# Kernel tuning notes

Measured on AMD Instinct MI355X. Metric: run time of the kernel, lower is better.

## Reference

```python
import jax, jax.numpy as jnp
import numpy as np

N, E, D, H, DH, M = 100000, 1600000, 128, 8, 16, 3  # nodes, edges, model_dim, heads, head_dim, views
NEG = -1e9


def setup_inputs() -> dict:
    key = jax.random.key(0)
    ks = jax.random.split(key, 12)
    x = jax.random.normal(ks[0], (N, D), jnp.float32)
    src = jax.random.randint(ks[1], (E,), 0, N)
    dst = jax.random.randint(ks[2], (E,), 0, N)
    pi = jax.random.uniform(ks[3], (N, H, M), jnp.float32)
    pi = pi / pi.sum(-1, keepdims=True)  # router mixture over views
    view_w = jax.random.uniform(ks[4], (E, M), jnp.float32)
    s = 1.0 / np.sqrt(D)
    Wq = jax.random.normal(ks[5], (D, D), jnp.float32) * s
    Wk = jax.random.normal(ks[6], (D, D), jnp.float32) * s
    Wv = jax.random.normal(ks[7], (D, D), jnp.float32) * s
    bq = jax.random.normal(ks[8], (D,), jnp.float32) * 0.02
    bk = jax.random.normal(ks[9], (D,), jnp.float32) * 0.02
    bv = jax.random.normal(ks[10], (D,), jnp.float32) * 0.02
    return {"x": x, "pi": pi, "view_w": view_w, "Wq": Wq, "bq": bq,
            "Wk": Wk, "bk": bk, "Wv": Wv, "bv": bv, "src": src, "dst": dst}


def reference(x, pi, view_w, Wq, bq, Wk, bk, Wv, bv, src, dst):
    n = x.shape[0]
    q = (x @ Wq + bq).reshape(n, H, DH)
    k = (x @ Wk + bk).reshape(n, H, DH)
    v = (x @ Wv + bv).reshape(n, H, DH)
    # per-edge mixture weight: sum over views of pi[dst] * view_w  -> [E, H]
    mix = jnp.einsum('ehm,em->eh', pi[dst], view_w)
    raw = jnp.einsum('ehd,ehd->eh', q[dst], k[src]) / jnp.sqrt(jnp.float32(DH))
    scores = raw + jnp.log(jnp.clip(mix, 1e-8))  # adjacency_mode == 'bias'
    valid = mix > 0
    masked = jnp.where(valid, scores, NEG)
    # scatter-softmax over incoming edges per (node, head)
    smax = jax.ops.segment_max(masked, dst, num_segments=n)
    expv = jnp.where(valid, jnp.exp(masked - smax[dst]), 0.0)
    ssum = jax.ops.segment_sum(expv, dst, num_segments=n)
    attn = expv / jnp.maximum(ssum[dst], 1e-8)  # [E, H]
    # weighted scatter-sum aggregation -> [N, H, DH]
    node_states = jax.ops.segment_sum(v[src] * attn[:, :, None], dst, num_segments=n)
    return node_states, attn
```

## Files before the change

kernel.cpp:

```cpp
#include <hip/hip_runtime.h>
#include <hip/hip_bf16.h>
#include <math.h>

#define SCAN_CHUNK 2048

typedef _Float16 half2v __attribute__((ext_vector_type(2)));
typedef _Float16 half8 __attribute__((ext_vector_type(8)));
typedef float floatx4 __attribute__((ext_vector_type(4)));

#if defined(__has_builtin)
#if __has_builtin(__builtin_amdgcn_fdot2)
#define USE_FDOT2 1
#endif
#endif


__global__ void hist_kernel(const int* __restrict__ dst, int* __restrict__ counts, int e) {
    int i = blockIdx.x * blockDim.x + threadIdx.x;
    if (i < e) atomicAdd(&counts[dst[i]], 1);
}

__global__ __launch_bounds__(256) void scan_block_sums(const int* __restrict__ counts,
                                                       int* __restrict__ bsum, int n) {
    __shared__ int sd[256];
    int t = threadIdx.x;
    int base = blockIdx.x * SCAN_CHUNK + t * 8;
    int s = 0;
#pragma unroll
    for (int j = 0; j < 8; ++j) {
        int idx = base + j;
        if (idx < n) s += counts[idx];
    }
    sd[t] = s;
    __syncthreads();
    for (int off = 128; off > 0; off >>= 1) {
        if (t < off) sd[t] += sd[t + off];
        __syncthreads();
    }
    if (t == 0) bsum[blockIdx.x] = sd[0];
}

__global__ void scan_wave(int* bsum, int nb) {
    int lane = threadIdx.x;
    int orig = (lane < nb) ? bsum[lane] : 0;
    int v = orig;
    for (int off = 1; off < 64; off <<= 1) {
        int t = __shfl_up(v, off, 64);
        if (lane >= off) v += t;
    }
    if (lane < nb) bsum[lane] = v - orig;
}

__global__ __launch_bounds__(256) void scan_write(const int* __restrict__ counts,
                                                  const int* __restrict__ bsum,
                                                  int* __restrict__ row_ptr,
                                                  int* __restrict__ cursor,
                                                  int n, int total) {
    __shared__ int sd[256];
    int t = threadIdx.x;
    int base = blockIdx.x * SCAN_CHUNK + t * 8;
    int v[8];
    int s = 0;
#pragma unroll
    for (int j = 0; j < 8; ++j) {
        int idx = base + j;
        v[j] = (idx < n) ? counts[idx] : 0;
        s += v[j];
    }
    sd[t] = s;
    __syncthreads();
    for (int off = 1; off < 256; off <<= 1) {
        int tmp = 0;
        if (t >= off) tmp = sd[t - off];
        __syncthreads();
        if (t >= off) sd[t] += tmp;
        __syncthreads();
    }
    int run = bsum[blockIdx.x] + sd[t] - s;
#pragma unroll
    for (int j = 0; j < 8; ++j) {
        int idx = base + j;
        if (idx < n) {
            row_ptr[idx] = run;
            cursor[idx] = run;
            run += v[j];
        }
    }
    if (blockIdx.x == 0 && t == 0) row_ptr[n] = total;
}

__global__ void fill_csr(const int* __restrict__ dst, const int* __restrict__ src,
                         const float* __restrict__ vw, int* cursor,
                         int4* __restrict__ recs, int* __restrict__ pos, int e) {
    int i = blockIdx.x * blockDim.x + threadIdx.x;
    if (i < e) {
        int p = atomicAdd(&cursor[dst[i]], 1);
        float w0 = vw[3 * i], w1 = vw[3 * i + 1], w2 = vw[3 * i + 2];
        unsigned u0 = (unsigned)__builtin_bit_cast(unsigned short, (_Float16)w0);
        unsigned u1 = (unsigned)__builtin_bit_cast(unsigned short, (_Float16)w1);
        unsigned u2 = (unsigned)__builtin_bit_cast(unsigned short, (_Float16)w2);
        int4 r;
        r.x = src[i];
        r.y = (int)u2;
        r.z = (int)(u0 | (u1 << 16));
        r.w = 0;
        recs[p] = r;
        pos[i] = p;
    }
}


__global__ __launch_bounds__(256) void convert_x(const float* __restrict__ x,
                                                 _Float16* __restrict__ xh, int total8) {
    int i = blockIdx.x * blockDim.x + threadIdx.x;
    if (i < total8) {
        const float4* s = (const float4*)x + i * 2;
        float4 a = s[0], b = s[1];
        half8 h;
        h[0] = (_Float16)a.x; h[1] = (_Float16)a.y; h[2] = (_Float16)a.z; h[3] = (_Float16)a.w;
        h[4] = (_Float16)b.x; h[5] = (_Float16)b.y; h[6] = (_Float16)b.z; h[7] = (_Float16)b.w;
        *((half8*)xh + i) = h;
    }
}

__global__ __launch_bounds__(256) void prep_w(const float* __restrict__ Wq,
                                              const float* __restrict__ Wk,
                                              const float* __restrict__ Wv,
                                              _Float16* __restrict__ wt) {
    const float* W = (blockIdx.x == 0) ? Wq : (blockIdx.x == 1) ? Wk : Wv;
    _Float16* out = wt + (size_t)blockIdx.x * 16384;
    int t = threadIdx.x;
    for (int r = 0; r < 64; ++r) {
        int idx = r * 256 + t;
        int k = idx >> 7, nn = idx & 127;
        out[nn * 128 + k] = (_Float16)W[idx];
    }
}


#define LDP 136

__global__ __launch_bounds__(256) void qkv_mfma(
    const _Float16* __restrict__ xh, const _Float16* __restrict__ wt,
    const float* __restrict__ bq, const float* __restrict__ bk,
    const float* __restrict__ bv,
    _Float16* __restrict__ qh, _Float16* __restrict__ kh, _Float16* __restrict__ vh,
    int n) {
    __shared__ __align__(16) _Float16 xs[128 * LDP];
    __shared__ __align__(16) _Float16 ws[128 * LDP];

    int t = threadIdx.x;
    int tile0 = blockIdx.x * 128;
    int sel = blockIdx.y;
    const _Float16* wsel = wt + (size_t)sel * 16384;
    const float* bias = (sel == 0) ? bq : (sel == 1) ? bk : bv;
    _Float16* out = (sel == 0) ? qh : (sel == 1) ? kh : vh;

#pragma unroll
    for (int r = 0; r < 8; ++r) {
        int id = r * 256 + t;
        int row = id >> 4, c8 = id & 15;
        int grow = tile0 + row;
        half8 val = (half8)(_Float16)0;
        if (grow < n) val = *((const half8*)(xh + (size_t)grow * 128) + c8);
        *((half8*)(xs + row * LDP) + c8) = val;
        half8 wv = *((const half8*)(wsel + row * 128) + c8);
        *((half8*)(ws + row * LDP) + c8) = wv;
    }
    __syncthreads();

    int wave = t >> 6, lane = t & 63;
    int wm = (wave & 1) * 64, wn = (wave >> 1) * 64;
    int lrow = lane & 15, quad = lane >> 4;

    floatx4 acc[4][4];
#pragma unroll
    for (int i = 0; i < 4; ++i)
#pragma unroll
        for (int j = 0; j < 4; ++j) acc[i][j] = (floatx4)0.f;

#pragma unroll
    for (int kk = 0; kk < 4; ++kk) {
        int kbase = kk * 32 + quad * 8;
        half8 a[4], b[4];
#pragma unroll
        for (int i = 0; i < 4; ++i)
            a[i] = *(const half8*)(xs + (wm + i * 16 + lrow) * LDP + kbase);
#pragma unroll
        for (int j = 0; j < 4; ++j)
            b[j] = *(const half8*)(ws + (wn + j * 16 + lrow) * LDP + kbase);
#pragma unroll
        for (int i = 0; i < 4; ++i)
#pragma unroll
            for (int j = 0; j < 4; ++j)
                acc[i][j] = __builtin_amdgcn_mfma_f32_16x16x32_f16(a[i], b[j], acc[i][j], 0, 0, 0);
    }

#pragma unroll
    for (int i = 0; i < 4; ++i) {
#pragma unroll
        for (int j = 0; j < 4; ++j) {
            int col = wn + j * 16 + lrow;
            float bv_ = bias[col];
#pragma unroll
            for (int r = 0; r < 4; ++r) {
                int row = wm + i * 16 + quad * 4 + r;
                int grow = tile0 + row;
                if (grow < n) out[(size_t)grow * 128 + col] = (_Float16)(acc[i][j][r] + bv_);
            }
        }
    }
}


#define STAGE_META(S, idx)                                                    \
    {                                                                         \
        s##S = 0; m##S = 0.f;                                                 \
        if ((idx) < end) {                                                    \
            int4 r_ = recs[(idx)];                                            \
            s##S = r_.x;                                                      \
            half2v w01_ = __builtin_bit_cast(half2v, r_.z);                   \
            _Float16 w2_ =                                                    \
                __builtin_bit_cast(_Float16, (unsigned short)(unsigned)r_.y); \
            m##S = fmaf(p0, (float)w01_[0],                                   \
                        fmaf(p1, (float)w01_[1], p2 * (float)w2_));           \
        }                                                                     \
    }

#define ISSUE_KV(S, idx)                                                      \
    {                                                                         \
        k##S = (half8)(_Float16)0; v##S = (half8)(_Float16)0;                 \
        if ((idx) < end) {                                                    \
            k##S = *(const half8*)(kbase + (size_t)s##S * 128);               \
            v##S = *(const half8*)(vbase + (size_t)s##S * 128);               \
        }                                                                     \
    }

#ifdef USE_FDOT2
#define DOT8(dres, kS)                                                        \
    {                                                                         \
        _Pragma("unroll")                                                     \
        for (int jj_ = 0; jj_ < 4; ++jj_) {                                   \
            half2v x_, y_;                                                    \
            x_[0] = qv[2 * jj_]; x_[1] = qv[2 * jj_ + 1];                     \
            y_[0] = kS[2 * jj_]; y_[1] = kS[2 * jj_ + 1];                     \
            dres = __builtin_amdgcn_fdot2(x_, y_, dres, false);               \
        }                                                                     \
    }
#else
#define DOT8(dres, kS)                                                        \
    {                                                                         \
        _Pragma("unroll")                                                     \
        for (int jj_ = 0; jj_ < 8; ++jj_)                                     \
            dres = fmaf((float)qv[jj_], (float)kS[jj_], dres);                \
    }
#endif

#define COMPUTE(S, mx, slot, validc)                                          \
    {                                                                         \
        float d_ = 0.f;                                                       \
        DOT8(d_, k##S);                                                       \
        d_ += __shfl_xor(d_, 1, 64);                                          \
        float p_ = ((mx) > 0.f) ? (mx)*__expf(d_ * 0.25f) : 0.f;              \
        if (sub == 0 && (validc)) pbuf[(size_t)(slot)*8 + h] = (_Float16)p_;  \
        l += p_;                                                              \
        a0 = fmaf(p_, (float)v##S[0], a0);                                    \
        a1 = fmaf(p_, (float)v##S[1], a1);                                    \
        a2 = fmaf(p_, (float)v##S[2], a2);                                    \
        a3 = fmaf(p_, (float)v##S[3], a3);                                    \
        a4 = fmaf(p_, (float)v##S[4], a4);                                    \
        a5 = fmaf(p_, (float)v##S[5], a5);                                    \
        a6 = fmaf(p_, (float)v##S[6], a6);                                    \
        a7 = fmaf(p_, (float)v##S[7], a7);                                    \
    }

#define BODY(S0, S1, S2, S3, jj)                                              \
    {                                                                         \
        ISSUE_KV(S2, (jj) + 2);                                               \
        ISSUE_KV(S3, (jj) + 3);                                               \
        float mx0_ = m##S0, mx1_ = m##S1;                                     \
        STAGE_META(S0, (jj) + 4);                                             \
        STAGE_META(S1, (jj) + 5);                                             \
        COMPUTE(S0, mx0_, (jj), true);                                        \
        COMPUTE(S1, mx1_, (jj) + 1, (jj) + 1 < end);                          \
    }

__global__ __launch_bounds__(64, 6) void edge_attn(
    const _Float16* __restrict__ qh, const _Float16* __restrict__ kh,
    const _Float16* __restrict__ vh, const float* __restrict__ pi,
    const int* __restrict__ row_ptr, const int4* __restrict__ recs,
    float* __restrict__ node_out, float* __restrict__ invb,
    _Float16* __restrict__ pbuf, int n) {
    int t = threadIdx.x;
    int node = blockIdx.x * 4 + (t >> 4);
    if (node >= n) return;
    int q16 = t & 15;
    int h = q16 >> 1, sub = q16 & 1;
    int off = h * 16 + sub * 8;

    const half8 qv = *(const half8*)(qh + (size_t)node * 128 + off);
    const _Float16* kbase = kh + off;
    const _Float16* vbase = vh + off;

    float p0 = pi[node * 24 + h * 3 + 0];
    float p1 = pi[node * 24 + h * 3 + 1];
    float p2 = pi[node * 24 + h * 3 + 2];
    int beg = row_ptr[node], end = row_ptr[node + 1];

    float l = 0.f;
    float a0 = 0.f, a1 = 0.f, a2 = 0.f, a3 = 0.f;
    float a4 = 0.f, a5 = 0.f, a6 = 0.f, a7 = 0.f;

    int sA, sB, sC, sD;
    float mA, mB, mC, mD;
    half8 kA, vA, kB, vB, kC, vC, kD, vD;

    STAGE_META(A, beg);
    STAGE_META(B, beg + 1);
    STAGE_META(C, beg + 2);
    STAGE_META(D, beg + 3);
    ISSUE_KV(A, beg);
    ISSUE_KV(B, beg + 1);

    for (int j = beg; j < end;) {
        BODY(A, B, C, D, j);
        j += 2;
        if (j >= end) break;
        BODY(C, D, A, B, j);
        j += 2;
    }

    float inv = 1.f / fmaxf(l, 1e-8f);
    if (sub == 0) invb[(size_t)node * 8 + h] = inv;

    float4* op = (float4*)(node_out + (size_t)node * 128 + off);
    op[0] = make_float4(a0 * inv, a1 * inv, a2 * inv, a3 * inv);
    op[1] = make_float4(a4 * inv, a5 * inv, a6 * inv, a7 * inv);
}


__global__ __launch_bounds__(256) void attn_norm(
    const _Float16* __restrict__ pbuf, const int* __restrict__ dst,
    const int* __restrict__ pos, const float* __restrict__ invb,
    float* __restrict__ attn_out, int e) {
    int i = blockIdx.x * blockDim.x + threadIdx.x;
    if (i < e) {
        int d = dst[i];
        int p = pos[i];
        half8 pv = *((const half8*)pbuf + p);
        const float4* iv = (const float4*)(invb + (size_t)d * 8);
        float4 i0 = iv[0], i1 = iv[1];
        float4* op = (float4*)(attn_out + (size_t)i * 8);
        op[0] = make_float4((float)pv[0] * i0.x, (float)pv[1] * i0.y,
                            (float)pv[2] * i0.z, (float)pv[3] * i0.w);
        op[1] = make_float4((float)pv[4] * i1.x, (float)pv[5] * i1.y,
                            (float)pv[6] * i1.z, (float)pv[7] * i1.w);
    }
}


extern "C" void kernel_launch(void* const* d_in, const int* in_sizes, int n_in,
                              void* d_out, int out_size, void* d_ws, size_t ws_size,
                              hipStream_t stream) {
    const float* x  = (const float*)d_in[0];
    const float* pi = (const float*)d_in[1];
    const float* vw = (const float*)d_in[2];
    const float* Wq = (const float*)d_in[3];
    const float* bq = (const float*)d_in[4];
    const float* Wk = (const float*)d_in[5];
    const float* bk = (const float*)d_in[6];
    const float* Wv = (const float*)d_in[7];
    const float* bv = (const float*)d_in[8];
    const int* src  = (const int*)d_in[9];
    const int* dst  = (const int*)d_in[10];

    int n = in_sizes[0] / 128;
    int e = in_sizes[9];

    _Float16* xh = (_Float16*)d_ws;
    _Float16* qh = xh + (size_t)n * 128;
    _Float16* kh = qh + (size_t)n * 128;
    _Float16* vh = kh + (size_t)n * 128;
    _Float16* wt = vh + (size_t)n * 128;
    _Float16* pbuf = wt + 3 * 16384;
    float* invb  = (float*)(pbuf + (size_t)e * 8);
    int* counts  = (int*)(invb + (size_t)n * 8);
    int* cursor  = counts + n;
    int* row_ptr = cursor + n;
    int* bsum    = row_ptr + n + 1;
    int* pos     = bsum + 64;

    float* node_out = (float*)d_out;
    float* attn_out = node_out + (size_t)n * 128;
    int4* recs = (int4*)attn_out;

    hipMemsetAsync(counts, 0, (size_t)n * sizeof(int), stream);

    int eb = (e + 255) / 256;
    hist_kernel<<<eb, 256, 0, stream>>>(dst, counts, e);

    int nb = (n + SCAN_CHUNK - 1) / SCAN_CHUNK;
    scan_block_sums<<<nb, 256, 0, stream>>>(counts, bsum, n);
    scan_wave<<<1, 64, 0, stream>>>(bsum, nb);
    scan_write<<<nb, 256, 0, stream>>>(counts, bsum, row_ptr, cursor, n, e);
    fill_csr<<<eb, 256, 0, stream>>>(dst, src, vw, cursor, recs, pos, e);

    int tot8 = (n * 128) / 8;
    convert_x<<<(tot8 + 255) / 256, 256, 0, stream>>>(x, xh, tot8);
    prep_w<<<3, 256, 0, stream>>>(Wq, Wk, Wv, wt);

    int gtiles = (n + 127) / 128;
    qkv_mfma<<<dim3(gtiles, 3), 256, 0, stream>>>(xh, wt, bq, bk, bv, qh, kh, vh, n);

    int gb = (n + 3) / 4;
    edge_attn<<<gb, 64, 0, stream>>>(qh, kh, vh, pi, row_ptr, recs,
                                     node_out, invb, pbuf, n);
    attn_norm<<<eb, 256, 0, stream>>>(pbuf, dst, pos, invb, attn_out, e);
}
```

Baseline: 619.1 us.

## Fuse x conversion into QKV GEMM and interleave K/V per head for edge gathers

Drops the separate fp32-to-fp16 conversion kernel: the QKV GEMM now reads fp32 x, converts it while staging to shared memory, and computes Q, K and V in one block by looping over the three weight matrices. K and V are written into one interleaved buffer (per head, K then V for 16 elements each), so each gathered edge fetches K and V from the same 64-byte region. The edge attention kernel also moves from 64-thread to 128-thread blocks covering 8 nodes. The cost is a 3x serial loop with extra barriers inside each GEMM block and fewer GEMM blocks overall.

```diff
diff --git a/kernel.cpp b/kernel.cpp
--- a/kernel.cpp
+++ b/kernel.cpp
@@ -109,20 +109,6 @@
     }
 }
 
-
-__global__ __launch_bounds__(256) void convert_x(const float* __restrict__ x,
-                                                 _Float16* __restrict__ xh, int total8) {
-    int i = blockIdx.x * blockDim.x + threadIdx.x;
-    if (i < total8) {
-        const float4* s = (const float4*)x + i * 2;
-        float4 a = s[0], b = s[1];
-        half8 h;
-        h[0] = (_Float16)a.x; h[1] = (_Float16)a.y; h[2] = (_Float16)a.z; h[3] = (_Float16)a.w;
-        h[4] = (_Float16)b.x; h[5] = (_Float16)b.y; h[6] = (_Float16)b.z; h[7] = (_Float16)b.w;
-        *((half8*)xh + i) = h;
-    }
-}
-
 __global__ __launch_bounds__(256) void prep_w(const float* __restrict__ Wq,
                                               const float* __restrict__ Wk,
                                               const float* __restrict__ Wv,
@@ -141,20 +127,15 @@
 #define LDP 136
 
 __global__ __launch_bounds__(256) void qkv_mfma(
-    const _Float16* __restrict__ xh, const _Float16* __restrict__ wt,
+    const float* __restrict__ x, const _Float16* __restrict__ wt,
     const float* __restrict__ bq, const float* __restrict__ bk,
     const float* __restrict__ bv,
-    _Float16* __restrict__ qh, _Float16* __restrict__ kh, _Float16* __restrict__ vh,
-    int n) {
+    _Float16* __restrict__ qh, _Float16* __restrict__ kvb, int n) {
     __shared__ __align__(16) _Float16 xs[128 * LDP];
     __shared__ __align__(16) _Float16 ws[128 * LDP];
 
     int t = threadIdx.x;
     int tile0 = blockIdx.x * 128;
-    int sel = blockIdx.y;
-    const _Float16* wsel = wt + (size_t)sel * 16384;
-    const float* bias = (sel == 0) ? bq : (sel == 1) ? bk : bv;
-    _Float16* out = (sel == 0) ? qh : (sel == 1) ? kh : vh;
 
 #pragma unroll
     for (int r = 0; r < 8; ++r) {
@@ -162,53 +143,80 @@
         int row = id >> 4, c8 = id & 15;
         int grow = tile0 + row;
         half8 val = (half8)(_Float16)0;
-        if (grow < n) val = *((const half8*)(xh + (size_t)grow * 128) + c8);
+        if (grow < n) {
+            const float4* s = (const float4*)(x + (size_t)grow * 128 + c8 * 8);
+            float4 a = s[0], b = s[1];
+            val[0] = (_Float16)a.x; val[1] = (_Float16)a.y;
+            val[2] = (_Float16)a.z; val[3] = (_Float16)a.w;
+            val[4] = (_Float16)b.x; val[5] = (_Float16)b.y;
+            val[6] = (_Float16)b.z; val[7] = (_Float16)b.w;
+        }
         *((half8*)(xs + row * LDP) + c8) = val;
-        half8 wv = *((const half8*)(wsel + row * 128) + c8);
-        *((half8*)(ws + row * LDP) + c8) = wv;
-    }
-    __syncthreads();
+    }
 
     int wave = t >> 6, lane = t & 63;
     int wm = (wave & 1) * 64, wn = (wave >> 1) * 64;
     int lrow = lane & 15, quad = lane >> 4;
 
-    floatx4 acc[4][4];
-#pragma unroll
-    for (int i = 0; i < 4; ++i)
-#pragma unroll
-        for (int j = 0; j < 4; ++j) acc[i][j] = (floatx4)0.f;
-
-#pragma unroll
-    for (int kk = 0; kk < 4; ++kk) {
-        int kbase = kk * 32 + quad * 8;
-        half8 a[4], b[4];
+    for (int sel = 0; sel < 3; ++sel) {
+        const _Float16* wsel = wt + (size_t)sel * 16384;
+        const float* bias = (sel == 0) ? bq : (sel == 1) ? bk : bv;
+
+#pragma unroll
+        for (int r = 0; r < 8; ++r) {
+            int id = r * 256 + t;
+            int row = id >> 4, c8 = id & 15;
+            half8 wv = *((const half8*)(wsel + row * 128) + c8);
+            *((half8*)(ws + row * LDP) + c8) = wv;
+        }
+        __syncthreads();
+
+        floatx4 acc[4][4];
 #pragma unroll
         for (int i = 0; i < 4; ++i)
-            a[i] = *(const half8*)(xs + (wm + i * 16 + lrow) * LDP + kbase);
-#pragma unroll
-        for (int j = 0; j < 4; ++j)
-            b[j] = *(const half8*)(ws + (wn + j * 16 + lrow) * LDP + kbase);
-#pragma unroll
-        for (int i = 0; i < 4; ++i)
+#pragma unroll
+            for (int j = 0; j < 4; ++j) acc[i][j] = (floatx4)0.f;
+
+#pragma unroll
+        for (int kk = 0; kk < 4; ++kk) {
+            int kbase = kk * 32 + quad * 8;
+            half8 a[4], b[4];
+#pragma unroll
+            for (int i = 0; i < 4; ++i)
+                a[i] = *(const half8*)(xs + (wm + i * 16 + lrow) * LDP + kbase);
 #pragma unroll
             for (int j = 0; j < 4; ++j)
-                acc[i][j] = __builtin_amdgcn_mfma_f32_16x16x32_f16(a[i], b[j], acc[i][j], 0, 0, 0);
-    }
-
-#pragma unroll
-    for (int i = 0; i < 4; ++i) {
-#pragma unroll
-        for (int j = 0; j < 4; ++j) {
-            int col = wn + j * 16 + lrow;
-            float bv_ = bias[col];
-#pragma unroll
-            for (int r = 0; r < 4; ++r) {
-                int row = wm + i * 16 + quad * 4 + r;
-                int grow = tile0 + row;
-                if (grow < n) out[(size_t)grow * 128 + col] = (_Float16)(acc[i][j][r] + bv_);
+                b[j] = *(const half8*)(ws + (wn + j * 16 + lrow) * LDP + kbase);
+#pragma unroll
+            for (int i = 0; i < 4; ++i)
+#pragma unroll
+                for (int j = 0; j < 4; ++j)
+                    acc[i][j] = __builtin_amdgcn_mfma_f32_16x16x32_f16(a[i], b[j], acc[i][j], 0, 0, 0);
+        }
+
+#pragma unroll
+        for (int i = 0; i < 4; ++i) {
+#pragma unroll
+            for (int j = 0; j < 4; ++j) {
+                int col = wn + j * 16 + lrow;
+                float bv_ = bias[col];
+                int h = col >> 4, dh = col & 15;
+#pragma unroll
+                for (int r = 0; r < 4; ++r) {
+                    int row = wm + i * 16 + quad * 4 + r;
+                    int grow = tile0 + row;
+                    if (grow < n) {
+                        _Float16 val = (_Float16)(acc[i][j][r] + bv_);
+                        if (sel == 0)
+                            qh[(size_t)grow * 128 + col] = val;
+                        else
+                            kvb[(size_t)grow * 256 + h * 32 + dh +
+                                (sel == 2 ? 16 : 0)] = val;
+                    }
+                }
             }
         }
+        __syncthreads();
     }
 }
 
@@ -231,8 +239,9 @@
     {                                                                         \
         k##S = (half8)(_Float16)0; v##S = (half8)(_Float16)0;                 \
         if ((idx) < end) {                                                    \
-            k##S = *(const half8*)(kbase + (size_t)s##S * 128);               \
-            v##S = *(const half8*)(vbase + (size_t)s##S * 128);               \
+            const _Float16* kp_ = kvbase + (size_t)s##S * 256;                \
+            k##S = *(const half8*)(kp_);                                      \
+            v##S = *(const half8*)(kp_ + 16);                                 \
         }                                                                     \
     }
 
@@ -285,22 +294,21 @@
         COMPUTE(S1, mx1_, (jj) + 1, (jj) + 1 < end);                          \
     }
 
-__global__ __launch_bounds__(64, 6) void edge_attn(
-    const _Float16* __restrict__ qh, const _Float16* __restrict__ kh,
-    const _Float16* __restrict__ vh, const float* __restrict__ pi,
+__global__ __launch_bounds__(128, 8) void edge_attn(
+    const _Float16* __restrict__ qh, const _Float16* __restrict__ kvb,
+    const float* __restrict__ pi,
     const int* __restrict__ row_ptr, const int4* __restrict__ recs,
     float* __restrict__ node_out, float* __restrict__ invb,
     _Float16* __restrict__ pbuf, int n) {
     int t = threadIdx.x;
-    int node = blockIdx.x * 4 + (t >> 4);
+    int node = blockIdx.x * 8 + (t >> 4);
     if (node >= n) return;
     int q16 = t & 15;
     int h = q16 >> 1, sub = q16 & 1;
     int off = h * 16 + sub * 8;
 
     const half8 qv = *(const half8*)(qh + (size_t)node * 128 + off);
-    const _Float16* kbase = kh + off;
-    const _Float16* vbase = vh + off;
+    const _Float16* kvbase = kvb + h * 32 + sub * 8;
 
     float p0 = pi[node * 24 + h * 3 + 0];
     float p1 = pi[node * 24 + h * 3 + 1];
@@ -377,11 +385,9 @@
     int n = in_sizes[0] / 128;
     int e = in_sizes[9];
 
-    _Float16* xh = (_Float16*)d_ws;
-    _Float16* qh = xh + (size_t)n * 128;
-    _Float16* kh = qh + (size_t)n * 128;
-    _Float16* vh = kh + (size_t)n * 128;
-    _Float16* wt = vh + (size_t)n * 128;
+    _Float16* qh  = (_Float16*)d_ws;
+    _Float16* kvb = qh + (size_t)n * 128;
+    _Float16* wt  = kvb + (size_t)n * 256;
     _Float16* pbuf = wt + 3 * 16384;
     float* invb  = (float*)(pbuf + (size_t)e * 8);
     int* counts  = (int*)(invb + (size_t)n * 8);
@@ -405,15 +411,13 @@
     scan_write<<<nb, 256, 0, stream>>>(counts, bsum, row_ptr, cursor, n, e);
     fill_csr<<<eb, 256, 0, stream>>>(dst, src, vw, cursor, recs, pos, e);
 
-    int tot8 = (n * 128) / 8;
-    convert_x<<<(tot8 + 255) / 256, 256, 0, stream>>>(x, xh, tot8);
     prep_w<<<3, 256, 0, stream>>>(Wq, Wk, Wv, wt);
 
     int gtiles = (n + 127) / 128;
-    qkv_mfma<<<dim3(gtiles, 3), 256, 0, stream>>>(xh, wt, bq, bk, bv, qh, kh, vh, n);
-
-    int gb = (n + 3) / 4;
-    edge_attn<<<gb, 64, 0, stream>>>(qh, kh, vh, pi, row_ptr, recs,
-                                     node_out, invb, pbuf, n);
+    qkv_mfma<<<gtiles, 256, 0, stream>>>(x, wt, bq, bk, bv, qh, kvb, n);
+
+    int gb = (n + 7) / 8;
+    edge_attn<<<gb, 128, 0, stream>>>(qh, kvb, pi, row_ptr, recs,
+                                      node_out, invb, pbuf, n);
     attn_norm<<<eb, 256, 0, stream>>>(pbuf, dst, pos, invb, attn_out, e);
 }
```

Measured after the change: 798.8 us. 1.29x slower.

## Interleave K and V per source node and use 4-lane-per-head edge attention

Applied to the files above, without the earlier changes.

The QKV GEMM now writes K and V into one interleaved buffer, so each lane fetches 4 K values and the matching 4 V values from one contiguous 16-byte chunk per gathered source node. The edge attention kernel goes from 2 to 4 lanes per head (128 threads per block, 32 per node), adds a second xor shuffle to finish the dot product, and deepens the KV prefetch from 2 to 4 edges ahead using six register stages. The goal is better gather coalescing and more memory-level parallelism for the random source-node reads. In exchange it uses twice as many threads, repeats the metadata loads and exp per lane, and adds scattered 2-byte stores in the GEMM epilogue.

```diff
diff --git a/kernel.cpp b/kernel.cpp
--- a/kernel.cpp
+++ b/kernel.cpp
@@ -5,6 +5,7 @@
 #define SCAN_CHUNK 2048
 
 typedef _Float16 half2v __attribute__((ext_vector_type(2)));
+typedef _Float16 half4v __attribute__((ext_vector_type(4)));
 typedef _Float16 half8 __attribute__((ext_vector_type(8)));
 typedef float floatx4 __attribute__((ext_vector_type(4)));
 
@@ -144,8 +145,7 @@
     const _Float16* __restrict__ xh, const _Float16* __restrict__ wt,
     const float* __restrict__ bq, const float* __restrict__ bk,
     const float* __restrict__ bv,
-    _Float16* __restrict__ qh, _Float16* __restrict__ kh, _Float16* __restrict__ vh,
-    int n) {
+    _Float16* __restrict__ qh, _Float16* __restrict__ kvb, int n) {
     __shared__ __align__(16) _Float16 xs[128 * LDP];
     __shared__ __align__(16) _Float16 ws[128 * LDP];
 
@@ -154,7 +154,6 @@
     int sel = blockIdx.y;
     const _Float16* wsel = wt + (size_t)sel * 16384;
     const float* bias = (sel == 0) ? bq : (sel == 1) ? bk : bv;
-    _Float16* out = (sel == 0) ? qh : (sel == 1) ? kh : vh;
 
 #pragma unroll
     for (int r = 0; r < 8; ++r) {
@@ -202,11 +201,20 @@
         for (int j = 0; j < 4; ++j) {
             int col = wn + j * 16 + lrow;
             float bv_ = bias[col];
+            int h = col >> 4, dh = col & 15;
+            int sub = dh >> 2, w = dh & 3;
 #pragma unroll
             for (int r = 0; r < 4; ++r) {
                 int row = wm + i * 16 + quad * 4 + r;
                 int grow = tile0 + row;
-                if (grow < n) out[(size_t)grow * 128 + col] = (_Float16)(acc[i][j][r] + bv_);
+                if (grow < n) {
+                    _Float16 val = (_Float16)(acc[i][j][r] + bv_);
+                    if (sel == 0)
+                        qh[(size_t)grow * 128 + col] = val;
+                    else
+                        kvb[(size_t)grow * 256 + h * 32 + sub * 8 +
+                            (sel == 2 ? 4 : 0) + w] = val;
+                }
             }
         }
     }
@@ -229,29 +237,28 @@
 
 #define ISSUE_KV(S, idx)                                                      \
     {                                                                         \
-        k##S = (half8)(_Float16)0; v##S = (half8)(_Float16)0;                 \
+        k##S = (half4v)(_Float16)0; v##S = (half4v)(_Float16)0;               \
         if ((idx) < end) {                                                    \
-            k##S = *(const half8*)(kbase + (size_t)s##S * 128);               \
-            v##S = *(const half8*)(vbase + (size_t)s##S * 128);               \
+            const _Float16* kp_ = kvbase + (size_t)s##S * 256;                \
+            k##S = *(const half4v*)(kp_);                                     \
+            v##S = *(const half4v*)(kp_ + 4);                                 \
         }                                                                     \
     }
 
 #ifdef USE_FDOT2
-#define DOT8(dres, kS)                                                        \
+#define DOT4(dres, kS)                                                        \
+    {                                                                         \
+        half2v x_, y_;                                                        \
+        x_[0] = qv[0]; x_[1] = qv[1]; y_[0] = kS[0]; y_[1] = kS[1];           \
+        dres = __builtin_amdgcn_fdot2(x_, y_, dres, false);                   \
+        x_[0] = qv[2]; x_[1] = qv[3]; y_[0] = kS[2]; y_[1] = kS[3];           \
+        dres = __builtin_amdgcn_fdot2(x_, y_, dres, false);                   \
+    }
+#else
+#define DOT4(dres, kS)                                                        \
     {                                                                         \
         _Pragma("unroll")                                                     \
-        for (int jj_ = 0; jj_ < 4; ++jj_) {                                   \
-            half2v x_, y_;                                                    \
-            x_[0] = qv[2 * jj_]; x_[1] = qv[2 * jj_ + 1];                     \
-            y_[0] = kS[2 * jj_]; y_[1] = kS[2 * jj_ + 1];                     \
-            dres = __builtin_amdgcn_fdot2(x_, y_, dres, false);               \
-        }                                                                     \
-    }
-#else
-#define DOT8(dres, kS)                                                        \
-    {                                                                         \
-        _Pragma("unroll")                                                     \
-        for (int jj_ = 0; jj_ < 8; ++jj_)                                     \
+        for (int jj_ = 0; jj_ < 4; ++jj_)                                     \
             dres = fmaf((float)qv[jj_], (float)kS[jj_], dres);                \
     }
 #endif
@@ -259,8 +266,9 @@
 #define COMPUTE(S, mx, slot, validc)                                          \
     {                                                                         \
         float d_ = 0.f;                                                       \
-        DOT8(d_, k##S);                                                       \
+        DOT4(d_, k##S);                                                       \
         d_ += __shfl_xor(d_, 1, 64);                                          \
+        d_ += __shfl_xor(d_, 2, 64);                                          \
         float p_ = ((mx) > 0.f) ? (mx)*__expf(d_ * 0.25f) : 0.f;              \
         if (sub == 0 && (validc)) pbuf[(size_t)(slot)*8 + h] = (_Float16)p_;  \
         l += p_;                                                              \
@@ -268,39 +276,34 @@
         a1 = fmaf(p_, (float)v##S[1], a1);                                    \
         a2 = fmaf(p_, (float)v##S[2], a2);                                    \
         a3 = fmaf(p_, (float)v##S[3], a3);                                    \
-        a4 = fmaf(p_, (float)v##S[4], a4);                                    \
-        a5 = fmaf(p_, (float)v##S[5], a5);                                    \
-        a6 = fmaf(p_, (float)v##S[6], a6);                                    \
-        a7 = fmaf(p_, (float)v##S[7], a7);                                    \
-    }
-
-#define BODY(S0, S1, S2, S3, jj)                                              \
-    {                                                                         \
-        ISSUE_KV(S2, (jj) + 2);                                               \
-        ISSUE_KV(S3, (jj) + 3);                                               \
+    }
+
+#define BODY(S0, S1, SI0, SI1, jj)                                            \
+    {                                                                         \
+        ISSUE_KV(SI0, (jj) + 4);                                              \
+        ISSUE_KV(SI1, (jj) + 5);                                              \
         float mx0_ = m##S0, mx1_ = m##S1;                                     \
-        STAGE_META(S0, (jj) + 4);                                             \
-        STAGE_META(S1, (jj) + 5);                                             \
+        STAGE_META(S0, (jj) + 6);                                             \
+        STAGE_META(S1, (jj) + 7);                                             \
         COMPUTE(S0, mx0_, (jj), true);                                        \
         COMPUTE(S1, mx1_, (jj) + 1, (jj) + 1 < end);                          \
     }
 
-__global__ __launch_bounds__(64, 6) void edge_attn(
-    const _Float16* __restrict__ qh, const _Float16* __restrict__ kh,
-    const _Float16* __restrict__ vh, const float* __restrict__ pi,
+__global__ __launch_bounds__(128, 6) void edge_attn(
+    const _Float16* __restrict__ qh, const _Float16* __restrict__ kvb,
+    const float* __restrict__ pi,
     const int* __restrict__ row_ptr, const int4* __restrict__ recs,
     float* __restrict__ node_out, float* __restrict__ invb,
     _Float16* __restrict__ pbuf, int n) {
     int t = threadIdx.x;
-    int node = blockIdx.x * 4 + (t >> 4);
+    int node = blockIdx.x * 4 + (t >> 5);
     if (node >= n) return;
-    int q16 = t & 15;
-    int h = q16 >> 1, sub = q16 & 1;
-    int off = h * 16 + sub * 8;
-
-    const half8 qv = *(const half8*)(qh + (size_t)node * 128 + off);
-    const _Float16* kbase = kh + off;
-    const _Float16* vbase = vh + off;
+    int q32 = t & 31;
+    int h = q32 >> 2, sub = q32 & 3;
+    int off = h * 16 + sub * 4;
+
+    const half4v qv = *(const half4v*)(qh + (size_t)node * 128 + off);
+    const _Float16* kvbase = kvb + h * 32 + sub * 8;
 
     float p0 = pi[node * 24 + h * 3 + 0];
     float p1 = pi[node * 24 + h * 3 + 1];
@@ -309,25 +312,31 @@
 
     float l = 0.f;
     float a0 = 0.f, a1 = 0.f, a2 = 0.f, a3 = 0.f;
-    float a4 = 0.f, a5 = 0.f, a6 = 0.f, a7 = 0.f;
-
-    int sA, sB, sC, sD;
-    float mA, mB, mC, mD;
-    half8 kA, vA, kB, vB, kC, vC, kD, vD;
+
+    int sA, sB, sC, sD, sE, sF;
+    float mA, mB, mC, mD, mE, mF;
+    half4v kA, vA, kB, vB, kC, vC, kD, vD, kE, vE, kF, vF;
 
     STAGE_META(A, beg);
     STAGE_META(B, beg + 1);
     STAGE_META(C, beg + 2);
     STAGE_META(D, beg + 3);
+    STAGE_META(E, beg + 4);
+    STAGE_META(F, beg + 5);
     ISSUE_KV(A, beg);
     ISSUE_KV(B, beg + 1);
+    ISSUE_KV(C, beg + 2);
+    ISSUE_KV(D, beg + 3);
 
     for (int j = beg; j < end;) {
-        BODY(A, B, C, D, j);
+        BODY(A, B, E, F, j);
         j += 2;
         if (j >= end) break;
         BODY(C, D, A, B, j);
         j += 2;
+        if (j >= end) break;
+        BODY(E, F, C, D, j);
+        j += 2;
     }
 
     float inv = 1.f / fmaxf(l, 1e-8f);
@@ -335,7 +344,6 @@
 
     float4* op = (float4*)(node_out + (size_t)node * 128 + off);
     op[0] = make_float4(a0 * inv, a1 * inv, a2 * inv, a3 * inv);
-    op[1] = make_float4(a4 * inv, a5 * inv, a6 * inv, a7 * inv);
 }
 
 
@@ -377,11 +385,10 @@
     int n = in_sizes[0] / 128;
     int e = in_sizes[9];
 
-    _Float16* xh = (_Float16*)d_ws;
-    _Float16* qh = xh + (size_t)n * 128;
-    _Float16* kh = qh + (size_t)n * 128;
-    _Float16* vh = kh + (size_t)n * 128;
-    _Float16* wt = vh + (size_t)n * 128;
+    _Float16* xh  = (_Float16*)d_ws;
+    _Float16* qh  = xh + (size_t)n * 128;
+    _Float16* kvb = qh + (size_t)n * 128;
+    _Float16* wt  = kvb + (size_t)n * 256;
     _Float16* pbuf = wt + 3 * 16384;
     float* invb  = (float*)(pbuf + (size_t)e * 8);
     int* counts  = (int*)(invb + (size_t)n * 8);
@@ -410,10 +417,10 @@
     prep_w<<<3, 256, 0, stream>>>(Wq, Wk, Wv, wt);
 
     int gtiles = (n + 127) / 128;
-    qkv_mfma<<<dim3(gtiles, 3), 256, 0, stream>>>(xh, wt, bq, bk, bv, qh, kh, vh, n);
+    qkv_mfma<<<dim3(gtiles, 3), 256, 0, stream>>>(xh, wt, bq, bk, bv, qh, kvb, n);
 
     int gb = (n + 3) / 4;
-    edge_attn<<<gb, 64, 0, stream>>>(qh, kh, vh, pi, row_ptr, recs,
-                                     node_out, invb, pbuf, n);
+    edge_attn<<<gb, 128, 0, stream>>>(qh, kvb, pi, row_ptr, recs,
+                                      node_out, invb, pbuf, n);
     attn_norm<<<eb, 256, 0, stream>>>(pbuf, dst, pos, invb, attn_out, e);
 }
```

Result: no change. 611.9 us (-1.2%).
